# Kernel tuning notes

Measured on AMD Instinct MI355X. Metric: run time of the kernel, lower is better.

The kernel has to match this reference:

```python
import jax, jax.numpy as jnp
import numpy as np

B, S, HID = 1, 2048, 2048
H, KV, D = 32, 8, 64          # num_heads, num_kv_heads, head_dim
N_REP = H // KV               # GQA groups = 4
FF = 8192
EPS = 1e-5
ROPE_THETA = 10000.0


def _rope_tables(seq_len, dim, dtype=jnp.float32):
    inv_freq = 1.0 / (ROPE_THETA ** (jnp.arange(0, dim, 2, dtype=jnp.float32) / dim))
    t = jnp.arange(seq_len, dtype=jnp.float32)
    freqs = jnp.outer(t, inv_freq)                 # [S, D/2]
    emb = jnp.concatenate([freqs, freqs], axis=-1) # [S, D]
    return jnp.cos(emb).astype(dtype)[None], jnp.sin(emb).astype(dtype)[None]  # [1,S,D]


def setup_inputs() -> dict:
    key = jax.random.key(0)
    ks = jax.random.split(key, 10)
    s = 0.02
    cos, sin = _rope_tables(S, D)
    return {
        "hidden_states": jax.random.normal(ks[0], (B, S, HID), jnp.float32),
        "cos": cos, "sin": sin,
        "wq": jax.random.normal(ks[1], (HID, H * D), jnp.float32) * s,
        "wk": jax.random.normal(ks[2], (HID, KV * D), jnp.float32) * s,
        "wv": jax.random.normal(ks[3], (HID, KV * D), jnp.float32) * s,
        "wo": jax.random.normal(ks[4], (H * D, HID), jnp.float32) * s,
        "w_ln1": jnp.ones((HID,), jnp.float32),
        "w_ln2": jnp.ones((HID,), jnp.float32),
        "w_gate": jax.random.normal(ks[5], (HID, FF), jnp.float32) * s,
        "w_up": jax.random.normal(ks[6], (HID, FF), jnp.float32) * s,
        "w_down": jax.random.normal(ks[7], (FF, HID), jnp.float32) * s,
    }


def _rmsnorm(x, w):
    var = jnp.mean(jnp.square(x), axis=-1, keepdims=True)
    return x * jax.lax.rsqrt(var + EPS) * w


def _rotate_half(x):
    x1, x2 = jnp.split(x, 2, axis=-1)
    return jnp.concatenate([-x2, x1], axis=-1)


def _apply_rope(q, k, cos, sin):
    # q,k: [B,H,S,D]; cos,sin: [B,S,D] -> unsqueeze head dim
    c, s = cos[:, None], sin[:, None]
    return q * c + _rotate_half(q) * s, k * c + _rotate_half(k) * s


def reference(hidden_states, cos, sin, wq, wk, wv, wo, w_ln1, w_ln2, w_gate, w_up, w_down):
    residual = hidden_states
    x = _rmsnorm(hidden_states, w_ln1)

    q = (x @ wq).reshape(B, S, H, D).transpose(0, 2, 1, 3)    # [B,H,S,D]
    k = (x @ wk).reshape(B, S, KV, D).transpose(0, 2, 1, 3)   # [B,KV,S,D]
    v = (x @ wv).reshape(B, S, KV, D).transpose(0, 2, 1, 3)
    q, k = _apply_rope(q, k, cos, sin)

    # repeat_kv (interleaved) for GQA
    k = jnp.repeat(k, N_REP, axis=1)                           # [B,H,S,D]
    v = jnp.repeat(v, N_REP, axis=1)

    scale = 1.0 / np.sqrt(D)
    scores = jnp.einsum("bhqd,bhkd->bhqk", q, k) * scale       # [B,H,S,S]
    causal = jnp.tril(jnp.ones((S, S), bool))
    scores = jnp.where(causal, scores, jnp.finfo(scores.dtype).min)
    probs = jax.nn.softmax(scores, axis=-1)
    attn = jnp.einsum("bhqk,bhkd->bhqd", probs, v)             # [B,H,S,D]
    attn = attn.transpose(0, 2, 1, 3).reshape(B, S, H * D)
    attn = attn @ wo

    h = residual + attn
    residual = h
    y = _rmsnorm(h, w_ln2)
    mlp = (jax.nn.silu(y @ w_gate) * (y @ w_up)) @ w_down
    return residual + mlp
```

## Files before the change

### kernel.cpp

```cpp
#include <hip/hip_runtime.h>
#include <hip/hip_bf16.h>
#include <cstdint>

#define S_LEN 2048
#define HIDN  2048
#define NH    32
#define NKV   8
#define HD    64
#define FFN   8192
#define QKVN  3072
#define QKVLD 3072

typedef __attribute__((ext_vector_type(4)))  float f32x4;
typedef __attribute__((ext_vector_type(16))) float f32x16;
typedef __attribute__((ext_vector_type(8)))  short short8;
typedef __attribute__((ext_vector_type(4)))  short s16x4;

__device__ __forceinline__ short f2bf(float f) {
  union { float f; uint32_t u; } v; v.f = f;
  uint32_t r = v.u + 0x7FFFu + ((v.u >> 16) & 1u);
  return (short)(r >> 16);
}
__device__ __forceinline__ float bf2f(short s) {
  union { float f; uint32_t u; } v; v.u = ((uint32_t)(uint16_t)s) << 16;
  return v.f;
}
__device__ __forceinline__ unsigned packbf2(float lo, float hi) {
  return (unsigned)(uint16_t)f2bf(lo) | ((unsigned)(uint16_t)f2bf(hi) << 16);
}

#define GLOAD_LDS16(gp, lp) \
  __builtin_amdgcn_global_load_lds((const __attribute__((address_space(1))) void*)(gp), \
                                   (__attribute__((address_space(3))) void*)(lp), 16, 0, 0)

#define BARRIER()  asm volatile("s_barrier" ::: "memory")
#define LGKM0()    asm volatile("s_waitcnt lgkmcnt(0)" ::: "memory")
#define SCHED0()   __builtin_amdgcn_sched_barrier(0)
#define VMCNT(N)   asm volatile("s_waitcnt vmcnt(%0)" :: "n"(N) : "memory")

__global__ __launch_bounds__(256) void convT_kernel(const float* __restrict__ src,
    short* __restrict__ dst, int K, int N) {
  __shared__ float t[64][65];
  const int k0 = blockIdx.x * 64, n0 = blockIdx.y * 64;
  const int tr = threadIdx.x >> 4, tc = (threadIdx.x & 15) * 4;
  #pragma unroll
  for (int i = 0; i < 4; ++i) {
    float4 v = *(const float4*)(src + (size_t)(k0 + tr + i * 16) * N + n0 + tc);
    t[tr + i * 16][tc] = v.x; t[tr + i * 16][tc + 1] = v.y;
    t[tr + i * 16][tc + 2] = v.z; t[tr + i * 16][tc + 3] = v.w;
  }
  __syncthreads();
  const int dr = threadIdx.x >> 2, dc = (threadIdx.x & 3) * 16;
  short8 o0, o1;
  #pragma unroll
  for (int j = 0; j < 8; ++j) { o0[j] = f2bf(t[dc + j][dr]); o1[j] = f2bf(t[dc + 8 + j][dr]); }
  short* dp = dst + (size_t)(n0 + dr) * K + k0 + dc;
  *(short8*)dp = o0;
  *(short8*)(dp + 8) = o1;
}

__global__ __launch_bounds__(256) void rmsnorm_kernel(const float* __restrict__ X,
    const float* __restrict__ W, short* __restrict__ Y) {
  int row = blockIdx.x;
  const float4* x4 = (const float4*)(X + (size_t)row * HIDN);
  const float4* w4 = (const float4*)W;
  float4 v0 = x4[2 * threadIdx.x];
  float4 v1 = x4[2 * threadIdx.x + 1];
  float ss = v0.x*v0.x + v0.y*v0.y + v0.z*v0.z + v0.w*v0.w
           + v1.x*v1.x + v1.y*v1.y + v1.z*v1.z + v1.w*v1.w;
  #pragma unroll
  for (int off = 32; off > 0; off >>= 1) ss += __shfl_xor(ss, off, 64);
  __shared__ float red[4];
  if ((threadIdx.x & 63) == 0) red[threadIdx.x >> 6] = ss;
  __syncthreads();
  ss = red[0] + red[1] + red[2] + red[3];
  float rs = rsqrtf(ss * (1.0f / HIDN) + 1e-5f);
  float4 w0 = w4[2 * threadIdx.x], w1 = w4[2 * threadIdx.x + 1];
  short8 o;
  o[0] = f2bf(v0.x * rs * w0.x); o[1] = f2bf(v0.y * rs * w0.y);
  o[2] = f2bf(v0.z * rs * w0.z); o[3] = f2bf(v0.w * rs * w0.w);
  o[4] = f2bf(v1.x * rs * w1.x); o[5] = f2bf(v1.y * rs * w1.y);
  o[6] = f2bf(v1.z * rs * w1.z); o[7] = f2bf(v1.w * rs * w1.w);
  *(short8*)(Y + (size_t)row * HIDN + threadIdx.x * 8) = o;
}

template<int EPI, int BN>
__global__ __launch_bounds__(512, 1) void gemm8p(const short* __restrict__ A,
    const short* __restrict__ BT, void* __restrict__ Cp, const void* __restrict__ Xp,
    int N, int Kfull, int KC, int gy) {
  constexpr int NFN = BN / 64;
  constexpr int LB  = BN / 128;
  constexpr int VN  = 2 + 2 * LB;
  __shared__ __align__(16) short As[2][256 * 64];
  __shared__ __align__(16) short Bs[2][BN * 64];
  const int tid = threadIdx.x, lane = tid & 63, w = tid >> 6;
  const int wm2 = w >> 2;
  const int wn = (w & 3) * (BN / 4);
  const int l15 = lane & 15, lg = lane >> 4;
  const int cpx = gy >> 3;
  const int xcd = blockIdx.x & 7, cid = blockIdx.x >> 3;
  const int by = xcd * cpx + cid % cpx, bx = cid / cpx;
  const int brow = bx * 256, bcol = by * BN;
  const size_t kbase = (size_t)blockIdx.z * KC;
  const int r8 = lane >> 3, c8 = lane & 7;
  const int gblk = c8 ^ r8;
  const int nt = KC / 64;
  f32x4 acc[8][NFN] = {};
  short8 af[4], bf[2][NFN];

  auto STA = [&](int p, int kt, int h) {
    const size_t kc = kbase + (size_t)kt * 64 + gblk * 8;
    #pragma unroll
    for (int j = 0; j < 2; ++j) {
      const short* g = A + (size_t)(brow + h * 128 + j * 64 + w * 8 + r8) * Kfull + kc;
      GLOAD_LDS16(g, &As[p][(h * 128 + j * 64 + w * 8) * 64]);
    }
  };
  auto STB = [&](int p, int kt, int h) {
    const size_t kc = kbase + (size_t)kt * 64 + gblk * 8;
    #pragma unroll
    for (int j = 0; j < LB; ++j) {
      const short* g = BT + (size_t)(bcol + h * (BN / 2) + j * 64 + w * 8 + r8) * Kfull + kc;
      GLOAD_LDS16(g, &Bs[p][(h * (BN / 2) + j * 64 + w * 8) * 64]);
    }
  };
  auto LDA = [&](int p, int mh, int kk) {
    #pragma unroll
    for (int m = 0; m < 4; ++m) {
      const int row = mh * 128 + wm2 * 64 + m * 16 + l15;
      af[m] = *(const short8*)&As[p][row * 64 + (((kk * 4 + lg) ^ (row & 7)) * 8)];
    }
  };
  auto LDB = [&](int p, int kk) {
    #pragma unroll
    for (int n = 0; n < NFN; ++n) {
      const int row = wn + n * 16 + l15;
      bf[kk][n] = *(const short8*)&Bs[p][row * 64 + (((kk * 4 + lg) ^ (row & 7)) * 8)];
    }
  };

#define MMQ(MH, KK) \
  __builtin_amdgcn_s_setprio(1); \
  _Pragma("unroll") \
  for (int m = 0; m < 4; ++m) \
    _Pragma("unroll") \
    for (int n = 0; n < NFN; ++n) \
      acc[(MH) * 4 + m][n] = __builtin_amdgcn_mfma_f32_16x16x32_bf16(af[m], bf[KK][n], acc[(MH) * 4 + m][n], 0, 0, 0); \
  __builtin_amdgcn_s_setprio(0);

  STB(0, 0, 0); STB(0, 0, 1); STA(0, 0, 0); STA(0, 0, 1);
  STB(1, 1, 0); STB(1, 1, 1); STA(1, 1, 0);
  VMCNT(VN);
  BARRIER();

  for (int i = 0; i < nt / 2; ++i) {
    const int t = 2 * i;
    const bool li = (i == nt / 2 - 1);
    LDA(0, 0, 0); LDB(0, 0); LDB(0, 1);
    STA(1, t + 1, 1);
    BARRIER(); LGKM0(); SCHED0();
    MMQ(0, 0);
    BARRIER();
    LDA(0, 0, 1);
    if (!li) STB(0, t + 2, 0);
    BARRIER(); LGKM0(); SCHED0();
    MMQ(0, 1);
    BARRIER();
    LDA(0, 1, 0);
    if (!li) STB(0, t + 2, 1);
    BARRIER(); LGKM0(); SCHED0();
    MMQ(1, 0);
    BARRIER();
    LDA(0, 1, 1);
    if (!li) STA(0, t + 2, 0);
    BARRIER(); LGKM0(); SCHED0();
    MMQ(1, 1);
    if (li) { VMCNT(0); } else { VMCNT(VN); }
    BARRIER();
    LDA(1, 0, 0); LDB(1, 0); LDB(1, 1);
    if (!li) STA(0, t + 2, 1);
    BARRIER(); LGKM0(); SCHED0();
    MMQ(0, 0);
    BARRIER();
    LDA(1, 0, 1);
    if (!li) STB(1, t + 3, 0);
    BARRIER(); LGKM0(); SCHED0();
    MMQ(0, 1);
    BARRIER();
    LDA(1, 1, 0);
    if (!li) STB(1, t + 3, 1);
    BARRIER(); LGKM0(); SCHED0();
    MMQ(1, 0);
    BARRIER();
    LDA(1, 1, 1);
    if (!li) STA(1, t + 3, 0);
    BARRIER(); LGKM0(); SCHED0();
    MMQ(1, 1);
    if (!li) { VMCNT(VN); }
    BARRIER();
  }
#undef MMQ

  #pragma unroll
  for (int mf = 0; mf < 8; ++mf) {
    const int r0 = brow + (mf >> 2) * 128 + wm2 * 64 + (mf & 3) * 16 + lg * 4;
    #pragma unroll
    for (int nf = 0; nf < NFN; ++nf) {
      const int c = bcol + wn + nf * 16 + l15;
      #pragma unroll
      for (int i4 = 0; i4 < 4; ++i4) {
        const size_t idx = (size_t)(r0 + i4) * N + c;
        float v = acc[mf][nf][i4];
        if (EPI == 0) ((short*)Cp)[idx] = f2bf(v);
        if (EPI == 2) {
          float gf = bf2f(((const short*)Xp)[idx]);
          ((short*)Cp)[idx] = f2bf(gf / (1.f + __expf(-gf)) * v);
        }
        if (EPI == 3) ((float*)Cp)[(size_t)blockIdx.z * S_LEN * N + idx] = v;
      }
    }
  }
}

template<int EPI>
__global__ __launch_bounds__(256) void gemm_bt(const short* __restrict__ A,
    const short* __restrict__ BT, void* __restrict__ Cp, const void* __restrict__ Xp,
    int M, int N, int Kfull, int KC, int gx) {
  __shared__ __align__(16) short Ass[128 * 64];
  __shared__ __align__(16) short Bss[128 * 64];
  const int tid = threadIdx.x, lane = tid & 63, w = tid >> 6;
  const int wm = (w >> 1) * 64, wn = (w & 1) * 64;
  const int l15 = lane & 15, lg = lane >> 4;
  const int nwg = gridDim.x;
  const int qq = nwg >> 3, xcd = blockIdx.x & 7, off = blockIdx.x >> 3;
  const int wg = xcd * qq + off;
  const int brow = (wg % gx) * 128, bcol = (wg / gx) * 128;
  const size_t kbase = (size_t)blockIdx.y * KC;
  const int srow8 = lane >> 3;
  const int gblk  = (lane & 7) ^ (srow8 & 7);
  f32x4 acc[4][4] = {};

  for (int k0 = 0; k0 < KC; k0 += 64) {
    #pragma unroll
    for (int j = 0; j < 4; ++j) {
      const int rbase = w * 32 + j * 8;
      const int row = rbase + srow8;
      const short* ga = A + (size_t)(brow + row) * Kfull + kbase + k0 + gblk * 8;
      GLOAD_LDS16(ga, Ass + rbase * 64);
      const short* gb = BT + (size_t)(bcol + row) * Kfull + kbase + k0 + gblk * 8;
      GLOAD_LDS16(gb, Bss + rbase * 64);
    }
    __syncthreads();
    #pragma unroll
    for (int kk = 0; kk < 2; ++kk) {
      short8 af[4], bf[4];
      #pragma unroll
      for (int m = 0; m < 4; ++m) {
        const int row = wm + m * 16 + l15;
        af[m] = *(const short8*)&Ass[row * 64 + (((kk * 4 + lg) ^ (l15 & 7)) * 8)];
      }
      #pragma unroll
      for (int n = 0; n < 4; ++n) {
        const int row = wn + n * 16 + l15;
        bf[n] = *(const short8*)&Bss[row * 64 + (((kk * 4 + lg) ^ (l15 & 7)) * 8)];
      }
      #pragma unroll
      for (int m = 0; m < 4; ++m)
        #pragma unroll
        for (int n = 0; n < 4; ++n)
          acc[m][n] = __builtin_amdgcn_mfma_f32_16x16x32_bf16(af[m], bf[n], acc[m][n], 0, 0, 0);
    }
    __syncthreads();
  }

  const int r0 = brow + wm + lg * 4;
  const int c0 = bcol + wn + l15;
  #pragma unroll
  for (int m = 0; m < 4; ++m)
    #pragma unroll
    for (int n = 0; n < 4; ++n)
      #pragma unroll
      for (int i = 0; i < 4; ++i) {
        const size_t idx = (size_t)(r0 + m * 16 + i) * N + (c0 + n * 16);
        float v = acc[m][n][i];
        if (EPI == 0) ((short*)Cp)[idx] = f2bf(v);
        if (EPI == 1) ((float*)Cp)[idx] = v + ((const float*)Xp)[idx];
        if (EPI == 2) {
          float gf = bf2f(((const short*)Xp)[idx]);
          ((short*)Cp)[idx] = f2bf(gf / (1.f + __expf(-gf)) * v);
        }
        if (EPI == 3) ((float*)Cp)[(size_t)blockIdx.y * M * N + idx] = v;
      }
}

__global__ __launch_bounds__(256) void rope_kernel(short* __restrict__ qkv,
    const float* __restrict__ cosb, const float* __restrict__ sinb) {
  int idx = blockIdx.x * 256 + threadIdx.x;
  int d = idx & 31;
  int hh = (idx >> 5) % (NH + NKV);
  int s = idx / (32 * (NH + NKV));
  int col = (hh < NH) ? hh * HD : HIDN + (hh - NH) * HD;
  short* base = qkv + (size_t)s * QKVLD + col;
  float c  = cosb[s * HD + d];
  float sn = sinb[s * HD + d];
  float x1 = bf2f(base[d]), x2 = bf2f(base[d + 32]);
  base[d]      = f2bf(x1 * c - x2 * sn);
  base[d + 32] = f2bf(x2 * c + x1 * sn);
}

__global__ __launch_bounds__(256) void attn_kernel(const short* __restrict__ QKV,
    short* __restrict__ O) {
  __shared__ __align__(16) short Ks[64][72];
  __shared__ __align__(16) short VTs[64][72];
  const int bid = blockIdx.x;
  const int half = bid >> 8, idx = bid & 255;
  const int h = idx & 31;
  int qt = idx >> 5;
  qt = half ? (15 - qt) : qt;
  const int kvh = h >> 2;
  const int tid = threadIdx.x, lane = tid & 63, w = tid >> 6;
  const int l31 = lane & 31, hi = lane >> 5;
  const int qb = qt * 128 + w * 32;
  const int kcol = HIDN + kvh * HD;
  const int vcol = HIDN + NKV * HD + kvh * HD;

  short8 Qr[4];
  {
    const short* qp = QKV + (size_t)(qb + l31) * QKVLD + h * HD;
    #pragma unroll
    for (int dk = 0; dk < 4; ++dk) {
      short8 qv = *(const short8*)(qp + dk * 16 + hi * 8);
      #pragma unroll
      for (int e = 0; e < 8; ++e) Qr[dk][e] = f2bf(bf2f(qv[e]) * 0.125f);
    }
  }
  float m_ = -3e38f, l_ = 0.f;
  f32x16 o0 = {}, o1 = {};
  const int nt = 2 * qt + 2;
  const int krow = tid >> 2, kcb = (tid & 3) * 16;
  const int vk = tid & 31, vdb = (tid >> 5) * 8;

  for (int t = 0; t < nt; ++t) {
    const int kb = t * 64;
    __syncthreads();
    {
      const short* gk = QKV + (size_t)(kb + krow) * QKVLD + kcol + kcb;
      short8 a = *(const short8*)gk;
      short8 b = *(const short8*)(gk + 8);
      *(short8*)&Ks[krow][kcb] = a;
      *(short8*)&Ks[krow][kcb + 8] = b;
    }
    #pragma unroll
    for (int i = 0; i < 2; ++i) {
      const int k = i * 32 + vk;
      short8 v = *(const short8*)(QKV + (size_t)(kb + k) * QKVLD + vcol + vdb);
      #pragma unroll
      for (int j = 0; j < 8; ++j) VTs[vdb + j][k] = v[j];
    }
    __syncthreads();
    if (kb < qb + 32) {
      f32x16 s[2] = {};
      #pragma unroll
      for (int kt = 0; kt < 2; ++kt)
        #pragma unroll
        for (int dk = 0; dk < 4; ++dk) {
          short8 kf = *(const short8*)&Ks[kt * 32 + l31][dk * 16 + hi * 8];
          s[kt] = __builtin_amdgcn_mfma_f32_32x32x16_bf16(kf, Qr[dk], s[kt], 0, 0, 0);
        }
      if (kb + 63 > qb) {
        const int qg = qb + l31;
        #pragma unroll
        for (int kt = 0; kt < 2; ++kt)
          #pragma unroll
          for (int r = 0; r < 16; ++r) {
            const int kg = kb + kt * 32 + (r & 3) + 8 * (r >> 2) + 4 * hi;
            if (kg > qg) s[kt][r] = -1e30f;
          }
      }
      float pm = s[0][0];
      #pragma unroll
      for (int r = 1; r < 16; ++r) pm = fmaxf(pm, s[0][r]);
      #pragma unroll
      for (int r = 0; r < 16; ++r) pm = fmaxf(pm, s[1][r]);
      pm = fmaxf(pm, __shfl_xor(pm, 32));
      const float mn = fmaxf(m_, pm);
      const float al = __expf(m_ - mn);
      float rsum = 0.f;
      #pragma unroll
      for (int kt = 0; kt < 2; ++kt)
        #pragma unroll
        for (int r = 0; r < 16; ++r) { s[kt][r] = __expf(s[kt][r] - mn); rsum += s[kt][r]; }
      rsum += __shfl_xor(rsum, 32);
      l_ = l_ * al + rsum;
      m_ = mn;
      o0 *= al; o1 *= al;
      unsigned wd[2][8], rw[2][8];
      #pragma unroll
      for (int kt = 0; kt < 2; ++kt)
        #pragma unroll
        for (int i = 0; i < 8; ++i) {
          wd[kt][i] = packbf2(s[kt][2 * i], s[kt][2 * i + 1]);
          rw[kt][i] = (unsigned)__shfl_xor((int)wd[kt][i], 32);
        }
      #pragma unroll
      for (int kt = 0; kt < 2; ++kt) {
        union { unsigned u[4]; short8 s8; } pf0, pf1;
        if (hi) {
          pf0.u[0] = rw[kt][2]; pf0.u[1] = rw[kt][3]; pf0.u[2] = wd[kt][2]; pf0.u[3] = wd[kt][3];
          pf1.u[0] = rw[kt][6]; pf1.u[1] = rw[kt][7]; pf1.u[2] = wd[kt][6]; pf1.u[3] = wd[kt][7];
        } else {
          pf0.u[0] = wd[kt][0]; pf0.u[1] = wd[kt][1]; pf0.u[2] = rw[kt][0]; pf0.u[3] = rw[kt][1];
          pf1.u[0] = wd[kt][4]; pf1.u[1] = wd[kt][5]; pf1.u[2] = rw[kt][4]; pf1.u[3] = rw[kt][5];
        }
        #pragma unroll
        for (int ks = 0; ks < 2; ++ks) {
          const short8 pB = ks ? pf1.s8 : pf0.s8;
          short8 va = *(const short8*)&VTs[l31][kt * 32 + ks * 16 + hi * 8];
          o0 = __builtin_amdgcn_mfma_f32_32x32x16_bf16(va, pB, o0, 0, 0, 0);
          short8 vb = *(const short8*)&VTs[32 + l31][kt * 32 + ks * 16 + hi * 8];
          o1 = __builtin_amdgcn_mfma_f32_32x32x16_bf16(vb, pB, o1, 0, 0, 0);
        }
      }
    }
  }
  const float inv = 1.f / l_;
  short* op = O + (size_t)(qb + l31) * HIDN + h * HD;
  #pragma unroll
  for (int dt = 0; dt < 2; ++dt) {
    const f32x16& o = dt ? o1 : o0;
    #pragma unroll
    for (int g = 0; g < 4; ++g) {
      s16x4 st;
      st[0] = f2bf(o[g * 4 + 0] * inv);
      st[1] = f2bf(o[g * 4 + 1] * inv);
      st[2] = f2bf(o[g * 4 + 2] * inv);
      st[3] = f2bf(o[g * 4 + 3] * inv);
      *(s16x4*)(op + dt * 32 + g * 8 + hi * 4) = st;
    }
  }
}

__global__ __launch_bounds__(256) void reduce_kernel(float* __restrict__ out,
    const float* __restrict__ P) {
  const size_t n = (size_t)S_LEN * HIDN;
  size_t i = ((size_t)blockIdx.x * 256 + threadIdx.x) * 4;
  float4 o = *(float4*)(out + i);
  float4 a = *(const float4*)(P + i);
  float4 b = *(const float4*)(P + n + i);
  o.x += a.x + b.x; o.y += a.y + b.y; o.z += a.z + b.z; o.w += a.w + b.w;
  *(float4*)(out + i) = o;
}

extern "C" void kernel_launch(void* const* d_in, const int* in_sizes, int n_in,
                              void* d_out, int out_size, void* d_ws, size_t ws_size,
                              hipStream_t stream) {
  const float* hs   = (const float*)d_in[0];
  const float* cosb = (const float*)d_in[1];
  const float* sinb = (const float*)d_in[2];
  const float* wq   = (const float*)d_in[3];
  const float* wk   = (const float*)d_in[4];
  const float* wv   = (const float*)d_in[5];
  const float* wo   = (const float*)d_in[6];
  const float* wln1 = (const float*)d_in[7];
  const float* wln2 = (const float*)d_in[8];
  const float* wg   = (const float*)d_in[9];
  const float* wu   = (const float*)d_in[10];
  const float* wd   = (const float*)d_in[11];
  float* out = (float*)d_out;
  char* ws = (char*)d_ws;
  const size_t MB = 1024 * 1024;
  short* xn    = (short*)(ws);
  short* y     = (short*)(ws + 8 * MB);
  short* attnO = (short*)(ws + 16 * MB);
  short* qkv   = (short*)(ws + 24 * MB);
  short* g     = (short*)(ws + 37 * MB);
  short* Wbuf  = (short*)(ws + 69 * MB);
  float* P     = (float*)(ws);

  convT_kernel<<<dim3(32, 32), 256, 0, stream>>>(wq, Wbuf, HIDN, NH * HD);
  convT_kernel<<<dim3(32, 8),  256, 0, stream>>>(wk, Wbuf + (size_t)2048 * HIDN, HIDN, NKV * HD);
  convT_kernel<<<dim3(32, 8),  256, 0, stream>>>(wv, Wbuf + (size_t)2560 * HIDN, HIDN, NKV * HD);
  rmsnorm_kernel<<<S_LEN, 256, 0, stream>>>(hs, wln1, xn);
  gemm8p<0, 128><<<dim3(192, 1, 1), 512, 0, stream>>>(xn, Wbuf, qkv, nullptr, QKVN, HIDN, HIDN, 24);
  convT_kernel<<<dim3(32, 32), 256, 0, stream>>>(wo, Wbuf, NH * HD, HIDN);
  rope_kernel<<<(S_LEN * (NH + NKV) * 32) / 256, 256, 0, stream>>>(qkv, cosb, sinb);
  attn_kernel<<<NH * (S_LEN / 128), 256, 0, stream>>>(qkv, attnO);
  gemm_bt<1><<<dim3(16 * 16, 1), 256, 0, stream>>>(attnO, Wbuf, out, hs, S_LEN, HIDN, NH * HD, NH * HD, 16);
  rmsnorm_kernel<<<S_LEN, 256, 0, stream>>>(out, wln2, y);
  convT_kernel<<<dim3(32, 128), 256, 0, stream>>>(wg, Wbuf, HIDN, FFN);
  gemm8p<0, 256><<<dim3(256, 1, 1), 512, 0, stream>>>(y, Wbuf, g, nullptr, FFN, HIDN, HIDN, 32);
  convT_kernel<<<dim3(32, 128), 256, 0, stream>>>(wu, Wbuf, HIDN, FFN);
  gemm8p<2, 256><<<dim3(256, 1, 1), 512, 0, stream>>>(y, Wbuf, g, g, FFN, HIDN, HIDN, 32);
  convT_kernel<<<dim3(128, 32), 256, 0, stream>>>(wd, Wbuf, FFN, HIDN);
  gemm8p<3, 128><<<dim3(128, 1, 2), 512, 0, stream>>>(g, Wbuf, P, nullptr, HIDN, FFN, FFN / 2, 16);
  reduce_kernel<<<(S_LEN * HIDN) / 1024, 256, 0, stream>>>(out, P);
}
```

Baseline: 463.7 us.

## Fuse gate and up GEMMs via interleaved weights; prefetch K/V in attention

The gate and up weights are transposed into one buffer with alternating 16-row groups. A single GEMM of width 2*FFN then computes both, and its epilogue applies SiLU(gate)*up directly. This drops the intermediate bf16 gate write and re-read, plus one kernel launch. The attention kernel now register-prefetches the next K/V tile while the current one is processed, and raises wave priority around the MFMA blocks. The workspace layout is reorganised so the separate weight buffers do not collide.

```diff
diff --git a/kernel.cpp b/kernel.cpp
--- a/kernel.cpp
+++ b/kernel.cpp
@@ -55,6 +55,29 @@
   #pragma unroll
   for (int j = 0; j < 8; ++j) { o0[j] = f2bf(t[dc + j][dr]); o1[j] = f2bf(t[dc + 8 + j][dr]); }
   short* dp = dst + (size_t)(n0 + dr) * K + k0 + dc;
+  *(short8*)dp = o0;
+  *(short8*)(dp + 8) = o1;
+}
+
+__global__ __launch_bounds__(256) void convT_pack_kernel(const float* __restrict__ src,
+    short* __restrict__ dst, int plane) {
+  __shared__ float t[64][65];
+  const int k0 = blockIdx.x * 64, n0 = blockIdx.y * 64;
+  const int tr = threadIdx.x >> 4, tc = (threadIdx.x & 15) * 4;
+  #pragma unroll
+  for (int i = 0; i < 4; ++i) {
+    float4 v = *(const float4*)(src + (size_t)(k0 + tr + i * 16) * FFN + n0 + tc);
+    t[tr + i * 16][tc] = v.x; t[tr + i * 16][tc + 1] = v.y;
+    t[tr + i * 16][tc + 2] = v.z; t[tr + i * 16][tc + 3] = v.w;
+  }
+  __syncthreads();
+  const int dr = threadIdx.x >> 2, dc = (threadIdx.x & 3) * 16;
+  const int n = n0 + dr;
+  const int rr = ((n >> 4) << 5) + plane * 16 + (n & 15);
+  short8 o0, o1;
+  #pragma unroll
+  for (int j = 0; j < 8; ++j) { o0[j] = f2bf(t[dc + j][dr]); o1[j] = f2bf(t[dc + 8 + j][dr]); }
+  short* dp = dst + (size_t)rr * HIDN + k0 + dc;
   *(short8*)dp = o0;
   *(short8*)(dp + 8) = o1;
 }
@@ -201,22 +224,40 @@
   }
 #undef MMQ
 
-  #pragma unroll
-  for (int mf = 0; mf < 8; ++mf) {
-    const int r0 = brow + (mf >> 2) * 128 + wm2 * 64 + (mf & 3) * 16 + lg * 4;
-    #pragma unroll
-    for (int nf = 0; nf < NFN; ++nf) {
-      const int c = bcol + wn + nf * 16 + l15;
-      #pragma unroll
-      for (int i4 = 0; i4 < 4; ++i4) {
-        const size_t idx = (size_t)(r0 + i4) * N + c;
-        float v = acc[mf][nf][i4];
-        if (EPI == 0) ((short*)Cp)[idx] = f2bf(v);
-        if (EPI == 2) {
-          float gf = bf2f(((const short*)Xp)[idx]);
-          ((short*)Cp)[idx] = f2bf(gf / (1.f + __expf(-gf)) * v);
-        }
-        if (EPI == 3) ((float*)Cp)[(size_t)blockIdx.z * S_LEN * N + idx] = v;
+  if (EPI == 4) {
+    const int No = N >> 1;
+    #pragma unroll
+    for (int mf = 0; mf < 8; ++mf) {
+      const int r0 = brow + (mf >> 2) * 128 + wm2 * 64 + (mf & 3) * 16 + lg * 4;
+      #pragma unroll
+      for (int jg = 0; jg < NFN / 2; ++jg) {
+        const int c = (bcol >> 1) + (wn >> 1) + jg * 16 + l15;
+        #pragma unroll
+        for (int i4 = 0; i4 < 4; ++i4) {
+          float gt = acc[mf][2 * jg][i4];
+          float up = acc[mf][2 * jg + 1][i4];
+          ((short*)Cp)[(size_t)(r0 + i4) * No + c] = f2bf(gt / (1.f + __expf(-gt)) * up);
+        }
+      }
+    }
+  } else {
+    #pragma unroll
+    for (int mf = 0; mf < 8; ++mf) {
+      const int r0 = brow + (mf >> 2) * 128 + wm2 * 64 + (mf & 3) * 16 + lg * 4;
+      #pragma unroll
+      for (int nf = 0; nf < NFN; ++nf) {
+        const int c = bcol + wn + nf * 16 + l15;
+        #pragma unroll
+        for (int i4 = 0; i4 < 4; ++i4) {
+          const size_t idx = (size_t)(r0 + i4) * N + c;
+          float v = acc[mf][nf][i4];
+          if (EPI == 0) ((short*)Cp)[idx] = f2bf(v);
+          if (EPI == 2) {
+            float gf = bf2f(((const short*)Xp)[idx]);
+            ((short*)Cp)[idx] = f2bf(gf / (1.f + __expf(-gf)) * v);
+          }
+          if (EPI == 3) ((float*)Cp)[(size_t)blockIdx.z * S_LEN * N + idx] = v;
+        }
       }
     }
   }
@@ -340,26 +381,35 @@
   const int krow = tid >> 2, kcb = (tid & 3) * 16;
   const int vk = tid & 31, vdb = (tid >> 5) * 8;
 
+  short8 kr0, kr1, vr0, vr1;
+  {
+    const short* gk = QKV + (size_t)krow * QKVLD + kcol + kcb;
+    kr0 = *(const short8*)gk; kr1 = *(const short8*)(gk + 8);
+    vr0 = *(const short8*)(QKV + (size_t)vk * QKVLD + vcol + vdb);
+    vr1 = *(const short8*)(QKV + (size_t)(32 + vk) * QKVLD + vcol + vdb);
+  }
+
   for (int t = 0; t < nt; ++t) {
     const int kb = t * 64;
-    __syncthreads();
-    {
-      const short* gk = QKV + (size_t)(kb + krow) * QKVLD + kcol + kcb;
-      short8 a = *(const short8*)gk;
-      short8 b = *(const short8*)(gk + 8);
-      *(short8*)&Ks[krow][kcb] = a;
-      *(short8*)&Ks[krow][kcb + 8] = b;
-    }
-    #pragma unroll
-    for (int i = 0; i < 2; ++i) {
-      const int k = i * 32 + vk;
-      short8 v = *(const short8*)(QKV + (size_t)(kb + k) * QKVLD + vcol + vdb);
-      #pragma unroll
-      for (int j = 0; j < 8; ++j) VTs[vdb + j][k] = v[j];
-    }
-    __syncthreads();
+    BARRIER();
+    *(short8*)&Ks[krow][kcb] = kr0;
+    *(short8*)&Ks[krow][kcb + 8] = kr1;
+    #pragma unroll
+    for (int j = 0; j < 8; ++j) VTs[vdb + j][vk] = vr0[j];
+    #pragma unroll
+    for (int j = 0; j < 8; ++j) VTs[vdb + j][32 + vk] = vr1[j];
+    LGKM0();
+    BARRIER();
+    if (t + 1 < nt) {
+      const int kb2 = kb + 64;
+      const short* gk = QKV + (size_t)(kb2 + krow) * QKVLD + kcol + kcb;
+      kr0 = *(const short8*)gk; kr1 = *(const short8*)(gk + 8);
+      vr0 = *(const short8*)(QKV + (size_t)(kb2 + vk) * QKVLD + vcol + vdb);
+      vr1 = *(const short8*)(QKV + (size_t)(kb2 + 32 + vk) * QKVLD + vcol + vdb);
+    }
     if (kb < qb + 32) {
       f32x16 s[2] = {};
+      __builtin_amdgcn_s_setprio(1);
       #pragma unroll
       for (int kt = 0; kt < 2; ++kt)
         #pragma unroll
@@ -367,6 +417,7 @@
           short8 kf = *(const short8*)&Ks[kt * 32 + l31][dk * 16 + hi * 8];
           s[kt] = __builtin_amdgcn_mfma_f32_32x32x16_bf16(kf, Qr[dk], s[kt], 0, 0, 0);
         }
+      __builtin_amdgcn_s_setprio(0);
       if (kb + 63 > qb) {
         const int qg = qb + l31;
         #pragma unroll
@@ -412,6 +463,7 @@
           pf0.u[0] = wd[kt][0]; pf0.u[1] = wd[kt][1]; pf0.u[2] = rw[kt][0]; pf0.u[3] = rw[kt][1];
           pf1.u[0] = wd[kt][4]; pf1.u[1] = wd[kt][5]; pf1.u[2] = rw[kt][4]; pf1.u[3] = rw[kt][5];
         }
+        __builtin_amdgcn_s_setprio(1);
         #pragma unroll
         for (int ks = 0; ks < 2; ++ks) {
           const short8 pB = ks ? pf1.s8 : pf0.s8;
@@ -420,6 +472,7 @@
           short8 vb = *(const short8*)&VTs[32 + l31][kt * 32 + ks * 16 + hi * 8];
           o1 = __builtin_amdgcn_mfma_f32_32x32x16_bf16(vb, pB, o1, 0, 0, 0);
         }
+        __builtin_amdgcn_s_setprio(0);
       }
     }
   }
@@ -469,29 +522,31 @@
   float* out = (float*)d_out;
   char* ws = (char*)d_ws;
   const size_t MB = 1024 * 1024;
-  short* xn    = (short*)(ws);
-  short* y     = (short*)(ws + 8 * MB);
-  short* attnO = (short*)(ws + 16 * MB);
-  short* qkv   = (short*)(ws + 24 * MB);
-  short* g     = (short*)(ws + 37 * MB);
-  short* Wbuf  = (short*)(ws + 69 * MB);
-  float* P     = (float*)(ws);
-
-  convT_kernel<<<dim3(32, 32), 256, 0, stream>>>(wq, Wbuf, HIDN, NH * HD);
-  convT_kernel<<<dim3(32, 8),  256, 0, stream>>>(wk, Wbuf + (size_t)2048 * HIDN, HIDN, NKV * HD);
-  convT_kernel<<<dim3(32, 8),  256, 0, stream>>>(wv, Wbuf + (size_t)2560 * HIDN, HIDN, NKV * HD);
+  short* Wbig  = (short*)(ws);
+  short* Wqkv  = Wbig;
+  short* xn    = (short*)(ws + 13 * MB);
+  short* qkv   = (short*)(ws + 21 * MB);
+  short* attnO = (short*)(ws + 34 * MB);
+  short* Wwo   = (short*)(ws + 42 * MB);
+  short* y     = (short*)(ws + 64 * MB);
+  short* g     = (short*)(ws + 72 * MB);
+  short* Wd    = Wbig;
+  float* P     = (float*)(ws + 32 * MB);
+
+  convT_kernel<<<dim3(32, 32), 256, 0, stream>>>(wq, Wqkv, HIDN, NH * HD);
+  convT_kernel<<<dim3(32, 8),  256, 0, stream>>>(wk, Wqkv + (size_t)2048 * HIDN, HIDN, NKV * HD);
+  convT_kernel<<<dim3(32, 8),  256, 0, stream>>>(wv, Wqkv + (size_t)2560 * HIDN, HIDN, NKV * HD);
   rmsnorm_kernel<<<S_LEN, 256, 0, stream>>>(hs, wln1, xn);
-  gemm8p<0, 128><<<dim3(192, 1, 1), 512, 0, stream>>>(xn, Wbuf, qkv, nullptr, QKVN, HIDN, HIDN, 24);
-  convT_kernel<<<dim3(32, 32), 256, 0, stream>>>(wo, Wbuf, NH * HD, HIDN);
+  gemm8p<0, 128><<<dim3(192, 1, 1), 512, 0, stream>>>(xn, Wqkv, qkv, nullptr, QKVN, HIDN, HIDN, 24);
+  convT_kernel<<<dim3(32, 32), 256, 0, stream>>>(wo, Wwo, NH * HD, HIDN);
   rope_kernel<<<(S_LEN * (NH + NKV) * 32) / 256, 256, 0, stream>>>(qkv, cosb, sinb);
   attn_kernel<<<NH * (S_LEN / 128), 256, 0, stream>>>(qkv, attnO);
-  gemm_bt<1><<<dim3(16 * 16, 1), 256, 0, stream>>>(attnO, Wbuf, out, hs, S_LEN, HIDN, NH * HD, NH * HD, 16);
+  gemm_bt<1><<<dim3(16 * 16, 1), 256, 0, stream>>>(attnO, Wwo, out, hs, S_LEN, HIDN, NH * HD, NH * HD, 16);
   rmsnorm_kernel<<<S_LEN, 256, 0, stream>>>(out, wln2, y);
-  convT_kernel<<<dim3(32, 128), 256, 0, stream>>>(wg, Wbuf, HIDN, FFN);
-  gemm8p<0, 256><<<dim3(256, 1, 1), 512, 0, stream>>>(y, Wbuf, g, nullptr, FFN, HIDN, HIDN, 32);
-  convT_kernel<<<dim3(32, 128), 256, 0, stream>>>(wu, Wbuf, HIDN, FFN);
-  gemm8p<2, 256><<<dim3(256, 1, 1), 512, 0, stream>>>(y, Wbuf, g, g, FFN, HIDN, HIDN, 32);
-  convT_kernel<<<dim3(128, 32), 256, 0, stream>>>(wd, Wbuf, FFN, HIDN);
-  gemm8p<3, 128><<<dim3(128, 1, 2), 512, 0, stream>>>(g, Wbuf, P, nullptr, HIDN, FFN, FFN / 2, 16);
+  convT_pack_kernel<<<dim3(32, 128), 256, 0, stream>>>(wg, Wbig, 0);
+  convT_pack_kernel<<<dim3(32, 128), 256, 0, stream>>>(wu, Wbig, 1);
+  gemm8p<4, 256><<<dim3(512, 1, 1), 512, 0, stream>>>(y, Wbig, g, nullptr, 2 * FFN, HIDN, HIDN, 64);
+  convT_kernel<<<dim3(128, 32), 256, 0, stream>>>(wd, Wd, FFN, HIDN);
+  gemm8p<3, 128><<<dim3(128, 1, 2), 512, 0, stream>>>(g, Wd, P, nullptr, HIDN, FFN, FFN / 2, 16);
   reduce_kernel<<<(S_LEN * HIDN) / 1024, 256, 0, stream>>>(out, P);
 }
```

Measured after the change: 438.6 us. 1.06x faster.
